# Kernel tuning notes

Measured on AMD Instinct MI355X. Metric: run time of the kernel, lower is better.

The kernel has to match this reference:

```python
import jax, jax.numpy as jnp
import numpy as np

B, C, H, W_ = 64, 512, 32, 32


def setup_inputs() -> dict:
    key = jax.random.key(0)
    k0, k1, k2, k3 = jax.random.split(key, 4)
    x = jax.random.normal(k0, (B, C, H, W_), dtype=jnp.float32)
    # conv1x1 weight [3c, c] (kernel dims of size 1 squeezed)
    W = jax.random.normal(k1, (3 * C, C), dtype=jnp.float32) * 0.02
    rel_h = jax.random.normal(k2, (1, C, H, 1), dtype=jnp.float32)
    rel_w = jax.random.normal(k3, (1, C, 1, W_), dtype=jnp.float32)
    return {"x": x, "W": W, "rel_h": rel_h, "rel_w": rel_w}


def reference(x, W, rel_h, rel_w):
    b, c, h, w = x.shape
    n = h * w
    xf = x.reshape(b, c, n)
    # 1x1 conv == channel matmul: [b, 3c, n]
    qkv = jnp.einsum('oc,bcn->bon', W, xf)
    q, k, v = jnp.split(qkv, 3, axis=1)  # each [b, c, n]
    # content-content: q^T k -> [b, n, n]
    content_content = jnp.einsum('bcn,bcm->bnm', q, k)
    # relative position bias: pos [c, n]; pos^T @ q -> [b, n, n]
    pos = (rel_h + rel_w).reshape(c, n)
    content_position = jnp.einsum('cn,bcm->bnm', pos, q)
    attention = jax.nn.softmax(content_content + content_position, axis=-1)
    # out = bmm(v, attention^T) -> [b, c, n]
    out = jnp.einsum('bcm,bnm->bcn', v, attention)
    return out.reshape(b, c, h, w)
```

## Files before the change

kernel.cpp:

```cpp
#include <hip/hip_runtime.h>

#define B_    64
#define C_    512
#define H_    32
#define WDIM  32
#define N_    1024
#define M3C   1536

typedef unsigned short ushort_t;
typedef __attribute__((ext_vector_type(8))) short bf16x8;
typedef __attribute__((ext_vector_type(4))) float f32x4;
typedef __attribute__((ext_vector_type(16))) float f32x16;

#define MEMFENCE asm volatile("" ::: "memory")

__device__ __forceinline__ ushort_t f2bf(float x) {
    unsigned u = __float_as_uint(x);
    unsigned r = (u + 0x7FFFu + ((u >> 16) & 1u)) >> 16;
    return (ushort_t)r;
}
__device__ __forceinline__ float bf2f(ushort_t b) {
    return __uint_as_float(((unsigned)b) << 16);
}
__device__ __forceinline__ void split_write(float v, ushort_t* __restrict__ ph,
                                            ushort_t* __restrict__ pl, size_t idx) {
    ushort_t hb = f2bf(v);
    ph[idx] = hb;
    pl[idx] = f2bf(v - bf2f(hb));
}

__device__ __forceinline__ void gld16(const void* g, void* l) {
    __builtin_amdgcn_global_load_lds((const __attribute__((address_space(1))) unsigned int*)g,
                                     (__attribute__((address_space(3))) unsigned int*)l,
                                     16, 0, 0);
}

__global__ __launch_bounds__(256) void pos_kernel(const float* __restrict__ rel_h,
                                                  const float* __restrict__ rel_w,
                                                  float* __restrict__ pos) {
    int idx = blockIdx.x * 256 + threadIdx.x;
    if (idx >= C_ * N_) return;
    int c = idx >> 10;
    int n = idx & (N_ - 1);
    int h = n >> 5;
    int w = n & (WDIM - 1);
    pos[idx] = rel_h[c * H_ + h] + rel_w[c * WDIM + w];
}

__global__ __launch_bounds__(256) void mmT_f32(const float* __restrict__ A, int lda,
                                               const float* __restrict__ B, int ldb,
                                               float* __restrict__ D, int ldd, int K) {
    __shared__ float As[16][64];
    __shared__ float Bs[16][64];
    const int m0 = blockIdx.y * 64;
    const int n0 = blockIdx.x * 64;
    const int tx = threadIdx.x, ty = threadIdx.y;
    const int tid = ty * 16 + tx;
    float acc[4][4] = {};
    for (int k0 = 0; k0 < K; k0 += 16) {
        #pragma unroll
        for (int t = 0; t < 4; ++t) {
            int e = tid + t * 256;
            int j = e >> 6, i = e & 63;
            As[j][i] = A[(size_t)(k0 + j) * lda + m0 + i];
            Bs[j][i] = B[(size_t)(k0 + j) * ldb + n0 + i];
        }
        __syncthreads();
        #pragma unroll
        for (int kk = 0; kk < 16; ++kk) {
            float a[4], bb[4];
            #pragma unroll
            for (int i = 0; i < 4; ++i) a[i]  = As[kk][ty * 4 + i];
            #pragma unroll
            for (int j = 0; j < 4; ++j) bb[j] = Bs[kk][tx * 4 + j];
            #pragma unroll
            for (int i = 0; i < 4; ++i)
                #pragma unroll
                for (int j = 0; j < 4; ++j)
                    acc[i][j] += a[i] * bb[j];
        }
        __syncthreads();
    }
    #pragma unroll
    for (int i = 0; i < 4; ++i)
        #pragma unroll
        for (int j = 0; j < 4; ++j)
            D[(size_t)(m0 + ty * 4 + i) * ldd + n0 + tx * 4 + j] = acc[i][j];
}

__global__ __launch_bounds__(256) void f_split(const float* __restrict__ Mtmp,
                                               const float* __restrict__ Wm,
                                               ushort_t* __restrict__ Fh,
                                               ushort_t* __restrict__ Fl) {
    int idx = blockIdx.x * 256 + threadIdx.x;
    if (idx >= 1024 * C_) return;
    int o = idx >> 9;
    int c = idx & (C_ - 1);
    float v = (o < 512) ? Mtmp[idx] : Wm[(size_t)(512 + o) * C_ + c];
    split_write(v, Fh, Fl, idx);
}

__global__ __launch_bounds__(256) void xT_split(const float* __restrict__ x,
                                                ushort_t* __restrict__ xh,
                                                ushort_t* __restrict__ xl) {
    __shared__ float t[32][33];
    const int bl = blockIdx.z;
    const int c0 = blockIdx.y * 32;
    const int n0 = blockIdx.x * 32;
    const float* xb = x + (size_t)bl * C_ * N_;
    ushort_t* xhb = xh + (size_t)bl * N_ * C_;
    ushort_t* xlb = xl + (size_t)bl * N_ * C_;
    const int tx = threadIdx.x & 31, ty = threadIdx.x >> 5;
    #pragma unroll
    for (int r = 0; r < 4; ++r)
        t[ty + r * 8][tx] = xb[(size_t)(c0 + ty + r * 8) * N_ + n0 + tx];
    __syncthreads();
    #pragma unroll
    for (int r = 0; r < 4; ++r) {
        float v = t[tx][ty + r * 8];
        size_t o = (size_t)(n0 + ty + r * 8) * C_ + c0 + tx;
        split_write(v, xhb, xlb, o);
    }
}


__global__ __launch_bounds__(512, 2) void g1_mfma(const ushort_t* __restrict__ Fh_,
                                                  const ushort_t* __restrict__ Fl_,
                                                  const ushort_t* __restrict__ xTh_,
                                                  const ushort_t* __restrict__ xTl_,
                                                  ushort_t* __restrict__ tTh_,
                                                  ushort_t* __restrict__ tTl_,
                                                  ushort_t* __restrict__ vh_,
                                                  ushort_t* __restrict__ vl_) {
    __shared__ ushort_t lds[2][4][2][4096];
    const int bl = blockIdx.z;
    const int n0 = blockIdx.x * 256;
    const int m0 = blockIdx.y * 256;
    const char* Ah = (const char*)Fh_;
    const char* Al = (const char*)Fl_;
    const char* Bh = (const char*)(xTh_ + (size_t)bl * N_ * C_);
    const char* Bl = (const char*)(xTl_ + (size_t)bl * N_ * C_);

    const int tid = threadIdx.x;
    const int lane = tid & 63, wid = tid >> 6;
    const int wr = wid >> 2, wc = wid & 3;
    const int l31 = lane & 31, l5 = lane >> 5;
    const int swz4 = (l31 >> 1) & 3;
    const int chk0 = ((l5)     ^ swz4) << 3;
    const int chk1 = ((2 | l5) ^ swz4) << 3;
    const int srow = tid >> 2;
    const int toff = srow * 1024 + (((tid & 3) ^ ((srow >> 1) & 3)) << 4);
    const int ldst = wid * 512;

    f32x16 acc[4][2] = {};

#define G1_ISSUE(buf, kb) \
    gld16(Ah + (size_t)(m0)       * 1024 + (kb) + toff, &lds[buf][0][0][ldst]); \
    gld16(Ah + (size_t)(m0 + 128) * 1024 + (kb) + toff, &lds[buf][0][1][ldst]); \
    gld16(Al + (size_t)(m0)       * 1024 + (kb) + toff, &lds[buf][1][0][ldst]); \
    gld16(Al + (size_t)(m0 + 128) * 1024 + (kb) + toff, &lds[buf][1][1][ldst]); \
    gld16(Bh + (size_t)(n0)       * 1024 + (kb) + toff, &lds[buf][2][0][ldst]); \
    gld16(Bh + (size_t)(n0 + 128) * 1024 + (kb) + toff, &lds[buf][2][1][ldst]); \
    gld16(Bl + (size_t)(n0)       * 1024 + (kb) + toff, &lds[buf][3][0][ldst]); \
    gld16(Bl + (size_t)(n0 + 128) * 1024 + (kb) + toff, &lds[buf][3][1][ldst]);

    G1_ISSUE(0, 0);
    G1_ISSUE(1, 64);
    int cur = 0;
    for (int t = 0; t < 16; ++t) {
        if (t + 1 < 16) asm volatile("s_waitcnt vmcnt(8)" ::: "memory");
        else            asm volatile("s_waitcnt vmcnt(0)" ::: "memory");
        __builtin_amdgcn_s_barrier();
        MEMFENCE;
        bf16x8 bh[2][2], bo[2][2];
        #pragma unroll
        for (int j = 0; j < 2; ++j) {
            int br = ((wc & 1) * 64 + j * 32 + l31) * 32;
            bh[j][0] = *(const bf16x8*)&lds[cur][2][wc >> 1][br + chk0];
            bh[j][1] = *(const bf16x8*)&lds[cur][2][wc >> 1][br + chk1];
            bo[j][0] = *(const bf16x8*)&lds[cur][3][wc >> 1][br + chk0];
            bo[j][1] = *(const bf16x8*)&lds[cur][3][wc >> 1][br + chk1];
        }
        #pragma unroll
        for (int i = 0; i < 4; ++i) {
            int ar = (i * 32 + l31) * 32;
            bf16x8 ah0 = *(const bf16x8*)&lds[cur][0][wr][ar + chk0];
            bf16x8 ah1 = *(const bf16x8*)&lds[cur][0][wr][ar + chk1];
            bf16x8 al0 = *(const bf16x8*)&lds[cur][1][wr][ar + chk0];
            bf16x8 al1 = *(const bf16x8*)&lds[cur][1][wr][ar + chk1];
            __builtin_amdgcn_s_setprio(1);
            #pragma unroll
            for (int j = 0; j < 2; ++j) {
                acc[i][j] = __builtin_amdgcn_mfma_f32_32x32x16_bf16(ah0, bh[j][0], acc[i][j], 0,0,0);
                acc[i][j] = __builtin_amdgcn_mfma_f32_32x32x16_bf16(ah0, bo[j][0], acc[i][j], 0,0,0);
                acc[i][j] = __builtin_amdgcn_mfma_f32_32x32x16_bf16(al0, bh[j][0], acc[i][j], 0,0,0);
                acc[i][j] = __builtin_amdgcn_mfma_f32_32x32x16_bf16(ah1, bh[j][1], acc[i][j], 0,0,0);
                acc[i][j] = __builtin_amdgcn_mfma_f32_32x32x16_bf16(ah1, bo[j][1], acc[i][j], 0,0,0);
                acc[i][j] = __builtin_amdgcn_mfma_f32_32x32x16_bf16(al1, bh[j][1], acc[i][j], 0,0,0);
            }
            __builtin_amdgcn_s_setprio(0);
        }
        asm volatile("s_waitcnt lgkmcnt(0)" ::: "memory");
        __builtin_amdgcn_sched_barrier(0);
        __builtin_amdgcn_s_barrier();
        MEMFENCE;
        if (t + 2 < 16) { G1_ISSUE(cur, (t + 2) * 64); }
        cur ^= 1;
    }
#undef G1_ISSUE

    if (m0 < 512) {
        ushort_t* th = tTh_ + (size_t)bl * N_ * C_;
        ushort_t* tl = tTl_ + (size_t)bl * N_ * C_;
        #pragma unroll
        for (int i = 0; i < 4; ++i)
            #pragma unroll
            for (int j = 0; j < 2; ++j) {
                int n = n0 + wc * 64 + j * 32 + l31;
                #pragma unroll
                for (int q = 0; q < 4; ++q) {
                    int o = m0 + wr * 128 + i * 32 + q * 8 + l5 * 4;
                    ushort4 h4, l4;
                    ushort_t hb;
                    float v0 = acc[i][j][q*4+0], v1 = acc[i][j][q*4+1];
                    float v2 = acc[i][j][q*4+2], v3 = acc[i][j][q*4+3];
                    hb = f2bf(v0); h4.x = hb; l4.x = f2bf(v0 - bf2f(hb));
                    hb = f2bf(v1); h4.y = hb; l4.y = f2bf(v1 - bf2f(hb));
                    hb = f2bf(v2); h4.z = hb; l4.z = f2bf(v2 - bf2f(hb));
                    hb = f2bf(v3); h4.w = hb; l4.w = f2bf(v3 - bf2f(hb));
                    *reinterpret_cast<ushort4*>(&th[(size_t)n * C_ + o]) = h4;
                    *reinterpret_cast<ushort4*>(&tl[(size_t)n * C_ + o]) = l4;
                }
            }
    } else {
        ushort_t* vh = vh_ + (size_t)bl * C_ * N_;
        ushort_t* vl = vl_ + (size_t)bl * C_ * N_;
        #pragma unroll
        for (int i = 0; i < 4; ++i)
            #pragma unroll
            for (int j = 0; j < 2; ++j) {
                int m = n0 + wc * 64 + j * 32 + l31;
                #pragma unroll
                for (int q = 0; q < 4; ++q) {
                    int cb = m0 - 512 + wr * 128 + i * 32 + q * 8 + l5 * 4;
                    #pragma unroll
                    for (int rr = 0; rr < 4; ++rr) {
                        float v = acc[i][j][q*4+rr];
                        ushort_t hb = f2bf(v);
                        vh[(size_t)(cb + rr) * N_ + m] = hb;
                        vl[(size_t)(cb + rr) * N_ + m] = f2bf(v - bf2f(hb));
                    }
                }
            }
    }
}

__global__ __launch_bounds__(512, 2) void g2_mfma(const ushort_t* __restrict__ xTh_,
                                                  const ushort_t* __restrict__ xTl_,
                                                  const ushort_t* __restrict__ rTh_,
                                                  const ushort_t* __restrict__ rTl_,
                                                  const ushort_t* __restrict__ tTh_,
                                                  const ushort_t* __restrict__ tTl_,
                                                  float* __restrict__ S) {
    __shared__ ushort_t lds[2][4][2][4096];
    const int bl = blockIdx.z;
    const int m0 = blockIdx.x * 256;
    const int n0 = blockIdx.y * 256;
    const char* xh = (const char*)(xTh_ + (size_t)bl * N_ * C_);
    const char* xl = (const char*)(xTl_ + (size_t)bl * N_ * C_);
    const char* th = (const char*)(tTh_ + (size_t)bl * N_ * C_);
    const char* tl = (const char*)(tTl_ + (size_t)bl * N_ * C_);
    const char* rh = (const char*)rTh_;
    const char* rl = (const char*)rTl_;

    const int tid = threadIdx.x;
    const int lane = tid & 63, wid = tid >> 6;
    const int wr = wid >> 2, wc = wid & 3;
    const int l31 = lane & 31, l5 = lane >> 5;
    const int swz4 = (l31 >> 1) & 3;
    const int chk0 = ((l5)     ^ swz4) << 3;
    const int chk1 = ((2 | l5) ^ swz4) << 3;
    const int srow = tid >> 2;
    const int toff = srow * 1024 + (((tid & 3) ^ ((srow >> 1) & 3)) << 4);
    const int ldst = wid * 512;

    f32x16 acc[4][2] = {};

#define G2_ISSUE(buf, pAh, pAl, pBh, pBl, kb) \
    gld16(pAh + (size_t)(n0)       * 1024 + (kb) + toff, &lds[buf][0][0][ldst]); \
    gld16(pAh + (size_t)(n0 + 128) * 1024 + (kb) + toff, &lds[buf][0][1][ldst]); \
    gld16(pAl + (size_t)(n0)       * 1024 + (kb) + toff, &lds[buf][1][0][ldst]); \
    gld16(pAl + (size_t)(n0 + 128) * 1024 + (kb) + toff, &lds[buf][1][1][ldst]); \
    gld16(pBh + (size_t)(m0)       * 1024 + (kb) + toff, &lds[buf][2][0][ldst]); \
    gld16(pBh + (size_t)(m0 + 128) * 1024 + (kb) + toff, &lds[buf][2][1][ldst]); \
    gld16(pBl + (size_t)(m0)       * 1024 + (kb) + toff, &lds[buf][3][0][ldst]); \
    gld16(pBl + (size_t)(m0 + 128) * 1024 + (kb) + toff, &lds[buf][3][1][ldst]);

    G2_ISSUE(0, xh, xl, th, tl, 0);
    G2_ISSUE(1, xh, xl, th, tl, 64);
    int cur = 0;
    for (int t = 0; t < 32; ++t) {
        if (t + 1 < 32) asm volatile("s_waitcnt vmcnt(8)" ::: "memory");
        else            asm volatile("s_waitcnt vmcnt(0)" ::: "memory");
        __builtin_amdgcn_s_barrier();
        MEMFENCE;
        bf16x8 bh[2][2], bo[2][2];
        #pragma unroll
        for (int j = 0; j < 2; ++j) {
            int br = ((wc & 1) * 64 + j * 32 + l31) * 32;
            bh[j][0] = *(const bf16x8*)&lds[cur][2][wc >> 1][br + chk0];
            bh[j][1] = *(const bf16x8*)&lds[cur][2][wc >> 1][br + chk1];
            bo[j][0] = *(const bf16x8*)&lds[cur][3][wc >> 1][br + chk0];
            bo[j][1] = *(const bf16x8*)&lds[cur][3][wc >> 1][br + chk1];
        }
        #pragma unroll
        for (int i = 0; i < 4; ++i) {
            int ar = (i * 32 + l31) * 32;
            bf16x8 ah0 = *(const bf16x8*)&lds[cur][0][wr][ar + chk0];
            bf16x8 ah1 = *(const bf16x8*)&lds[cur][0][wr][ar + chk1];
            bf16x8 al0 = *(const bf16x8*)&lds[cur][1][wr][ar + chk0];
            bf16x8 al1 = *(const bf16x8*)&lds[cur][1][wr][ar + chk1];
            __builtin_amdgcn_s_setprio(1);
            #pragma unroll
            for (int j = 0; j < 2; ++j) {
                acc[i][j] = __builtin_amdgcn_mfma_f32_32x32x16_bf16(ah0, bh[j][0], acc[i][j], 0,0,0);
                acc[i][j] = __builtin_amdgcn_mfma_f32_32x32x16_bf16(ah0, bo[j][0], acc[i][j], 0,0,0);
                acc[i][j] = __builtin_amdgcn_mfma_f32_32x32x16_bf16(al0, bh[j][0], acc[i][j], 0,0,0);
                acc[i][j] = __builtin_amdgcn_mfma_f32_32x32x16_bf16(ah1, bh[j][1], acc[i][j], 0,0,0);
                acc[i][j] = __builtin_amdgcn_mfma_f32_32x32x16_bf16(ah1, bo[j][1], acc[i][j], 0,0,0);
                acc[i][j] = __builtin_amdgcn_mfma_f32_32x32x16_bf16(al1, bh[j][1], acc[i][j], 0,0,0);
            }
            __builtin_amdgcn_s_setprio(0);
        }
        asm volatile("s_waitcnt lgkmcnt(0)" ::: "memory");
        __builtin_amdgcn_sched_barrier(0);
        __builtin_amdgcn_s_barrier();
        MEMFENCE;
        if (t + 2 < 32) {
            int s = t + 2;
            const char* pAh = (s < 16) ? xh : rh;
            const char* pAl = (s < 16) ? xl : rl;
            const char* pBh = (s < 16) ? th : xh;
            const char* pBl = (s < 16) ? tl : xl;
            int kb = (s & 15) * 64;
            G2_ISSUE(cur, pAh, pAl, pBh, pBl, kb);
        }
        cur ^= 1;
    }
#undef G2_ISSUE

    float* Sb = S + (size_t)bl * N_ * N_;
    #pragma unroll
    for (int i = 0; i < 4; ++i)
        #pragma unroll
        for (int j = 0; j < 2; ++j) {
            int m = m0 + wc * 64 + j * 32 + l31;
            #pragma unroll
            for (int q = 0; q < 4; ++q) {
                int n = n0 + wr * 128 + i * 32 + q * 8 + l5 * 4;
                #pragma unroll
                for (int rr = 0; rr < 4; ++rr)
                    Sb[(size_t)(n + rr) * N_ + m] = acc[i][j][q*4+rr];
            }
        }
}

__device__ __forceinline__ float waveMax(float v) {
    #pragma unroll
    for (int o = 32; o > 0; o >>= 1) v = fmaxf(v, __shfl_down(v, o));
    return v;
}
__device__ __forceinline__ float waveSum(float v) {
    #pragma unroll
    for (int o = 32; o > 0; o >>= 1) v += __shfl_down(v, o);
    return v;
}

__global__ __launch_bounds__(256) void softmax_bf16(const float* __restrict__ S,
                                                    ushort_t* __restrict__ P) {
    const float* Sr = S + (size_t)blockIdx.x * N_;
    ushort_t* Pr = P + (size_t)blockIdx.x * N_;
    const int tid = threadIdx.x;
    float4 v = reinterpret_cast<const float4*>(Sr)[tid];
    __shared__ float redm[4];
    __shared__ float reds[4];
    const int wave = tid >> 6, lane = tid & 63;

    float m = fmaxf(fmaxf(v.x, v.y), fmaxf(v.z, v.w));
    m = waveMax(m);
    if (lane == 0) redm[wave] = m;
    __syncthreads();
    m = fmaxf(fmaxf(redm[0], redm[1]), fmaxf(redm[2], redm[3]));

    v.x = __expf(v.x - m); v.y = __expf(v.y - m);
    v.z = __expf(v.z - m); v.w = __expf(v.w - m);
    float s = v.x + v.y + v.z + v.w;
    s = waveSum(s);
    if (lane == 0) reds[wave] = s;
    __syncthreads();
    s = reds[0] + reds[1] + reds[2] + reds[3];
    const float inv = 1.0f / s;
    ushort4 p;
    p.x = f2bf(v.x * inv); p.y = f2bf(v.y * inv);
    p.z = f2bf(v.z * inv); p.w = f2bf(v.w * inv);
    reinterpret_cast<ushort4*>(Pr)[tid] = p;
}

__global__ __launch_bounds__(512, 2) void g4_mfma(const ushort_t* __restrict__ vh_,
                                                  const ushort_t* __restrict__ vl_,
                                                  const ushort_t* __restrict__ P_,
                                                  float* __restrict__ out) {
    __shared__ ushort_t lds[2][3][2][4096];
    const int bl = blockIdx.z;
    const int n0 = blockIdx.x * 256;
    const int c0 = blockIdx.y * 256;
    const char* Ah = (const char*)(vh_ + (size_t)bl * C_ * N_);
    const char* Al = (const char*)(vl_ + (size_t)bl * C_ * N_);
    const char* Bp = (const char*)(P_ + (size_t)bl * N_ * N_);

    const int tid = threadIdx.x;
    const int lane = tid & 63, wid = tid >> 6;
    const int wr = wid >> 2, wc = wid & 3;
    const int l31 = lane & 31, l5 = lane >> 5;
    const int swz4 = (l31 >> 1) & 3;
    const int chk0 = ((l5)     ^ swz4) << 3;
    const int chk1 = ((2 | l5) ^ swz4) << 3;
    const int srow = tid >> 2;
    const int toff = srow * 2048 + (((tid & 3) ^ ((srow >> 1) & 3)) << 4);
    const int ldst = wid * 512;

    f32x16 acc[4][2] = {};

#define G4_ISSUE(buf, kb) \
    gld16(Ah + (size_t)(c0)       * 2048 + (kb) + toff, &lds[buf][0][0][ldst]); \
    gld16(Ah + (size_t)(c0 + 128) * 2048 + (kb) + toff, &lds[buf][0][1][ldst]); \
    gld16(Al + (size_t)(c0)       * 2048 + (kb) + toff, &lds[buf][1][0][ldst]); \
    gld16(Al + (size_t)(c0 + 128) * 2048 + (kb) + toff, &lds[buf][1][1][ldst]); \
    gld16(Bp + (size_t)(n0)       * 2048 + (kb) + toff, &lds[buf][2][0][ldst]); \
    gld16(Bp + (size_t)(n0 + 128) * 2048 + (kb) + toff, &lds[buf][2][1][ldst]);

    G4_ISSUE(0, 0);
    G4_ISSUE(1, 64);
    int cur = 0;
    for (int t = 0; t < 32; ++t) {
        if (t + 1 < 32) asm volatile("s_waitcnt vmcnt(6)" ::: "memory");
        else            asm volatile("s_waitcnt vmcnt(0)" ::: "memory");
        __builtin_amdgcn_s_barrier();
        MEMFENCE;
        bf16x8 bf[2][2];
        #pragma unroll
        for (int j = 0; j < 2; ++j) {
            int br = ((wc & 1) * 64 + j * 32 + l31) * 32;
            bf[j][0] = *(const bf16x8*)&lds[cur][2][wc >> 1][br + chk0];
            bf[j][1] = *(const bf16x8*)&lds[cur][2][wc >> 1][br + chk1];
        }
        #pragma unroll
        for (int i = 0; i < 4; ++i) {
            int ar = (i * 32 + l31) * 32;
            bf16x8 ah0 = *(const bf16x8*)&lds[cur][0][wr][ar + chk0];
            bf16x8 ah1 = *(const bf16x8*)&lds[cur][0][wr][ar + chk1];
            bf16x8 al0 = *(const bf16x8*)&lds[cur][1][wr][ar + chk0];
            bf16x8 al1 = *(const bf16x8*)&lds[cur][1][wr][ar + chk1];
            __builtin_amdgcn_s_setprio(1);
            #pragma unroll
            for (int j = 0; j < 2; ++j) {
                acc[i][j] = __builtin_amdgcn_mfma_f32_32x32x16_bf16(ah0, bf[j][0], acc[i][j], 0,0,0);
                acc[i][j] = __builtin_amdgcn_mfma_f32_32x32x16_bf16(al0, bf[j][0], acc[i][j], 0,0,0);
                acc[i][j] = __builtin_amdgcn_mfma_f32_32x32x16_bf16(ah1, bf[j][1], acc[i][j], 0,0,0);
                acc[i][j] = __builtin_amdgcn_mfma_f32_32x32x16_bf16(al1, bf[j][1], acc[i][j], 0,0,0);
            }
            __builtin_amdgcn_s_setprio(0);
        }
        asm volatile("s_waitcnt lgkmcnt(0)" ::: "memory");
        __builtin_amdgcn_sched_barrier(0);
        __builtin_amdgcn_s_barrier();
        MEMFENCE;
        if (t + 2 < 32) { G4_ISSUE(cur, (t + 2) * 64); }
        cur ^= 1;
    }
#undef G4_ISSUE

    float* ob = out + (size_t)bl * C_ * N_;
    #pragma unroll
    for (int i = 0; i < 4; ++i)
        #pragma unroll
        for (int j = 0; j < 2; ++j) {
            int n = n0 + wc * 64 + j * 32 + l31;
            #pragma unroll
            for (int q = 0; q < 4; ++q) {
                int c = c0 + wr * 128 + i * 32 + q * 8 + l5 * 4;
                #pragma unroll
                for (int rr = 0; rr < 4; ++rr)
                    ob[(size_t)(c + rr) * N_ + n] = acc[i][j][q*4+rr];
            }
        }
}

extern "C" void kernel_launch(void* const* d_in, const int* in_sizes, int n_in,
                              void* d_out, int out_size, void* d_ws, size_t ws_size,
                              hipStream_t stream) {
    const float* x     = (const float*)d_in[0];
    const float* Wm    = (const float*)d_in[1];
    const float* rel_h = (const float*)d_in[2];
    const float* rel_w = (const float*)d_in[3];
    float* out = (float*)d_out;

    const size_t posB  = (size_t)C_ * N_ * 4;
    const size_t MtB   = (size_t)C_ * C_ * 4;
    const size_t rtB   = (size_t)C_ * N_ * 4;
    const size_t fplB  = (size_t)1024 * C_ * 2;
    const size_t rtplB = (size_t)N_ * C_ * 2;
    const size_t xtB   = (size_t)N_ * C_ * 2;
    const size_t ttB   = (size_t)N_ * C_ * 2;
    const size_t vplB  = (size_t)C_ * N_ * 2;
    const size_t sB    = (size_t)N_ * N_ * 4;
    const size_t pB    = (size_t)N_ * N_ * 2;
    const size_t per_batch = 2 * xtB + 2 * ttB + 2 * vplB + sB + pB;
    const size_t persist   = posB + MtB + rtB + 2 * fplB + 2 * rtplB;

    size_t rem = (ws_size > persist) ? (ws_size - persist) : 0;
    int chunkB = (int)(rem / per_batch);
    if (chunkB < 1)  chunkB = 1;
    if (chunkB > B_) chunkB = B_;

    char* p = (char*)d_ws;
    float*    pos  = (float*)p;    p += posB;
    float*    Mtmp = (float*)p;    p += MtB;
    float*    rtmp = (float*)p;    p += rtB;
    ushort_t* Fh   = (ushort_t*)p; p += fplB;
    ushort_t* Fl   = (ushort_t*)p; p += fplB;
    ushort_t* rTh  = (ushort_t*)p; p += rtplB;
    ushort_t* rTl  = (ushort_t*)p; p += rtplB;
    ushort_t* xTh  = (ushort_t*)p; p += (size_t)chunkB * xtB;
    ushort_t* xTl  = (ushort_t*)p; p += (size_t)chunkB * xtB;
    ushort_t* tTh  = (ushort_t*)p; p += (size_t)chunkB * ttB;
    ushort_t* tTl  = (ushort_t*)p; p += (size_t)chunkB * ttB;
    ushort_t* vh   = (ushort_t*)p; p += (size_t)chunkB * vplB;
    ushort_t* vl   = (ushort_t*)p; p += (size_t)chunkB * vplB;
    float*    S    = (float*)p;    p += (size_t)chunkB * sB;
    ushort_t* P    = (ushort_t*)p; p += (size_t)chunkB * pB;

    dim3 blk16(16, 16);
    pos_kernel<<<(C_ * N_ + 255) / 256, 256, 0, stream>>>(rel_h, rel_w, pos);
    mmT_f32<<<dim3(C_ / 64, C_ / 64), blk16, 0, stream>>>(Wm, C_, Wm + (size_t)C_ * C_, C_,
                                                          Mtmp, C_, C_);
    mmT_f32<<<dim3(N_ / 64, C_ / 64), blk16, 0, stream>>>(Wm, C_, pos, N_, rtmp, N_, C_);
    f_split<<<(1024 * C_ + 255) / 256, 256, 0, stream>>>(Mtmp, Wm, Fh, Fl);
    xT_split<<<dim3(N_ / 32, C_ / 32, 1), 256, 0, stream>>>(rtmp, rTh, rTl);

    for (int b0 = 0; b0 < B_; b0 += chunkB) {
        int nb = (b0 + chunkB <= B_) ? chunkB : (B_ - b0);
        const float* x_b   = x   + (size_t)b0 * C_ * N_;
        float*       out_b = out + (size_t)b0 * C_ * N_;
        xT_split<<<dim3(N_ / 32, C_ / 32, nb), 256, 0, stream>>>(x_b, xTh, xTl);
        g1_mfma<<<dim3(4, 4, nb), 512, 0, stream>>>(Fh, Fl, xTh, xTl, tTh, tTl, vh, vl);
        g2_mfma<<<dim3(4, 4, nb), 512, 0, stream>>>(xTh, xTl, rTh, rTl, tTh, tTl, S);
        softmax_bf16<<<nb * N_, 256, 0, stream>>>(S, P);
        g4_mfma<<<dim3(4, 2, nb), 512, 0, stream>>>(vh, vl, P, out_b);
    }
}
```

Baseline: 1.332 ms.

## Restructure split-bf16 GEMM mainloops into 4-phase 128-wide-K pipeline with 16x16 MFMA

Rewrites the three split-precision GEMM kernels so each K step is 128 wide and is split into four quadrant phases. Each phase issues the next staging load (6 stages in flight) and then runs 16x16x32 MFMAs on one 128x128 quadrant. The hi/lo split terms are now serialised along the K dimension as segments instead of being issued as paired MFMAs. The goal is finer-grained overlap of global-to-LDS loads with compute and fewer barriers per FLOP, with an XOR swizzle over 8 chunks to avoid LDS bank conflicts. The costs are a more complex wait schedule and different MFMA shapes and accumulator layout.

Result: slower. 1.759 ms (+32.0%).

```diff
diff --git a/kernel.cpp b/kernel.cpp
--- a/kernel.cpp
+++ b/kernel.cpp
@@ -10,7 +10,6 @@
 typedef unsigned short ushort_t;
 typedef __attribute__((ext_vector_type(8))) short bf16x8;
 typedef __attribute__((ext_vector_type(4))) float f32x4;
-typedef __attribute__((ext_vector_type(16))) float f32x16;
 
 #define MEMFENCE asm volatile("" ::: "memory")
 
@@ -124,6 +123,49 @@
 }
 
 
+#define STAGE2(srcp, gstride, r0, kb, dstp) \
+    _Pragma("unroll") \
+    for (int s_ = 0; s_ < 2; ++s_) { \
+        int row_ = s_ * 64 + (tid >> 3); \
+        gld16((srcp) + (size_t)((r0) + row_) * (gstride) + (kb) + \
+                  (((tid & 7) ^ (row_ & 7)) << 4), \
+              (dstp) + s_ * 4096 + (wid << 9)); \
+    }
+
+#define PHASE_WAIT(t_, q_, TT) \
+    if ((t_) < (TT) - 1) asm volatile("s_waitcnt vmcnt(8)" ::: "memory"); \
+    else if ((q_) == 0)  asm volatile("s_waitcnt vmcnt(4)" ::: "memory"); \
+    else if ((q_) == 1)  asm volatile("s_waitcnt vmcnt(2)" ::: "memory"); \
+    else                 asm volatile("s_waitcnt vmcnt(0)" ::: "memory");
+
+#define PHASE_COMPUTE(buf_, qr_, qc_, q_) \
+    bf16x8 af_[4][2], bf_[2][2]; \
+    _Pragma("unroll") \
+    for (int i_ = 0; i_ < 4; ++i_) { \
+        int row_ = wr * 64 + i_ * 16 + lr; \
+        const ushort_t* ab_ = &ldsA[buf_][qr_][row_ * 64]; \
+        af_[i_][0] = *(const bf16x8*)&ab_[((g ^ (row_ & 7)) << 3)]; \
+        af_[i_][1] = *(const bf16x8*)&ab_[(((4 + g) ^ (row_ & 7)) << 3)]; \
+    } \
+    _Pragma("unroll") \
+    for (int j_ = 0; j_ < 2; ++j_) { \
+        int row_ = wc * 32 + j_ * 16 + lr; \
+        const ushort_t* bb_ = &ldsB[buf_][qc_][row_ * 64]; \
+        bf_[j_][0] = *(const bf16x8*)&bb_[((g ^ (row_ & 7)) << 3)]; \
+        bf_[j_][1] = *(const bf16x8*)&bb_[(((4 + g) ^ (row_ & 7)) << 3)]; \
+    } \
+    asm volatile("s_waitcnt lgkmcnt(0)" ::: "memory"); \
+    __builtin_amdgcn_sched_barrier(0); \
+    __builtin_amdgcn_s_setprio(1); \
+    _Pragma("unroll") \
+    for (int i_ = 0; i_ < 4; ++i_) \
+        _Pragma("unroll") \
+        for (int j_ = 0; j_ < 2; ++j_) { \
+            acc[q_][i_][j_] = __builtin_amdgcn_mfma_f32_16x16x32_bf16(af_[i_][0], bf_[j_][0], acc[q_][i_][j_], 0, 0, 0); \
+            acc[q_][i_][j_] = __builtin_amdgcn_mfma_f32_16x16x32_bf16(af_[i_][1], bf_[j_][1], acc[q_][i_][j_], 0, 0, 0); \
+        } \
+    __builtin_amdgcn_s_setprio(0);
+
 __global__ __launch_bounds__(512, 2) void g1_mfma(const ushort_t* __restrict__ Fh_,
                                                   const ushort_t* __restrict__ Fl_,
                                                   const ushort_t* __restrict__ xTh_,
@@ -132,98 +174,73 @@
                                                   ushort_t* __restrict__ tTl_,
                                                   ushort_t* __restrict__ vh_,
                                                   ushort_t* __restrict__ vl_) {
-    __shared__ ushort_t lds[2][4][2][4096];
+    __shared__ ushort_t ldsA[2][2][8192];
+    __shared__ ushort_t ldsB[2][2][8192];
     const int bl = blockIdx.z;
     const int n0 = blockIdx.x * 256;
     const int m0 = blockIdx.y * 256;
-    const char* Ah = (const char*)Fh_;
-    const char* Al = (const char*)Fl_;
-    const char* Bh = (const char*)(xTh_ + (size_t)bl * N_ * C_);
-    const char* Bl = (const char*)(xTl_ + (size_t)bl * N_ * C_);
+    const char* fh = (const char*)Fh_;
+    const char* fl = (const char*)Fl_;
+    const char* xh = (const char*)(xTh_ + (size_t)bl * N_ * C_);
+    const char* xl = (const char*)(xTl_ + (size_t)bl * N_ * C_);
 
     const int tid = threadIdx.x;
     const int lane = tid & 63, wid = tid >> 6;
     const int wr = wid >> 2, wc = wid & 3;
-    const int l31 = lane & 31, l5 = lane >> 5;
-    const int swz4 = (l31 >> 1) & 3;
-    const int chk0 = ((l5)     ^ swz4) << 3;
-    const int chk1 = ((2 | l5) ^ swz4) << 3;
-    const int srow = tid >> 2;
-    const int toff = srow * 1024 + (((tid & 3) ^ ((srow >> 1) & 3)) << 4);
-    const int ldst = wid * 512;
-
-    f32x16 acc[4][2] = {};
-
-#define G1_ISSUE(buf, kb) \
-    gld16(Ah + (size_t)(m0)       * 1024 + (kb) + toff, &lds[buf][0][0][ldst]); \
-    gld16(Ah + (size_t)(m0 + 128) * 1024 + (kb) + toff, &lds[buf][0][1][ldst]); \
-    gld16(Al + (size_t)(m0)       * 1024 + (kb) + toff, &lds[buf][1][0][ldst]); \
-    gld16(Al + (size_t)(m0 + 128) * 1024 + (kb) + toff, &lds[buf][1][1][ldst]); \
-    gld16(Bh + (size_t)(n0)       * 1024 + (kb) + toff, &lds[buf][2][0][ldst]); \
-    gld16(Bh + (size_t)(n0 + 128) * 1024 + (kb) + toff, &lds[buf][2][1][ldst]); \
-    gld16(Bl + (size_t)(n0)       * 1024 + (kb) + toff, &lds[buf][3][0][ldst]); \
-    gld16(Bl + (size_t)(n0 + 128) * 1024 + (kb) + toff, &lds[buf][3][1][ldst]);
-
-    G1_ISSUE(0, 0);
-    G1_ISSUE(1, 64);
-    int cur = 0;
-    for (int t = 0; t < 16; ++t) {
-        if (t + 1 < 16) asm volatile("s_waitcnt vmcnt(8)" ::: "memory");
-        else            asm volatile("s_waitcnt vmcnt(0)" ::: "memory");
-        __builtin_amdgcn_s_barrier();
-        MEMFENCE;
-        bf16x8 bh[2][2], bo[2][2];
-        #pragma unroll
-        for (int j = 0; j < 2; ++j) {
-            int br = ((wc & 1) * 64 + j * 32 + l31) * 32;
-            bh[j][0] = *(const bf16x8*)&lds[cur][2][wc >> 1][br + chk0];
-            bh[j][1] = *(const bf16x8*)&lds[cur][2][wc >> 1][br + chk1];
-            bo[j][0] = *(const bf16x8*)&lds[cur][3][wc >> 1][br + chk0];
-            bo[j][1] = *(const bf16x8*)&lds[cur][3][wc >> 1][br + chk1];
-        }
-        #pragma unroll
-        for (int i = 0; i < 4; ++i) {
-            int ar = (i * 32 + l31) * 32;
-            bf16x8 ah0 = *(const bf16x8*)&lds[cur][0][wr][ar + chk0];
-            bf16x8 ah1 = *(const bf16x8*)&lds[cur][0][wr][ar + chk1];
-            bf16x8 al0 = *(const bf16x8*)&lds[cur][1][wr][ar + chk0];
-            bf16x8 al1 = *(const bf16x8*)&lds[cur][1][wr][ar + chk1];
-            __builtin_amdgcn_s_setprio(1);
-            #pragma unroll
-            for (int j = 0; j < 2; ++j) {
-                acc[i][j] = __builtin_amdgcn_mfma_f32_32x32x16_bf16(ah0, bh[j][0], acc[i][j], 0,0,0);
-                acc[i][j] = __builtin_amdgcn_mfma_f32_32x32x16_bf16(ah0, bo[j][0], acc[i][j], 0,0,0);
-                acc[i][j] = __builtin_amdgcn_mfma_f32_32x32x16_bf16(al0, bh[j][0], acc[i][j], 0,0,0);
-                acc[i][j] = __builtin_amdgcn_mfma_f32_32x32x16_bf16(ah1, bh[j][1], acc[i][j], 0,0,0);
-                acc[i][j] = __builtin_amdgcn_mfma_f32_32x32x16_bf16(ah1, bo[j][1], acc[i][j], 0,0,0);
-                acc[i][j] = __builtin_amdgcn_mfma_f32_32x32x16_bf16(al1, bh[j][1], acc[i][j], 0,0,0);
-            }
-            __builtin_amdgcn_s_setprio(0);
-        }
-        asm volatile("s_waitcnt lgkmcnt(0)" ::: "memory");
-        __builtin_amdgcn_sched_barrier(0);
-        __builtin_amdgcn_s_barrier();
-        MEMFENCE;
-        if (t + 2 < 16) { G1_ISSUE(cur, (t + 2) * 64); }
-        cur ^= 1;
-    }
-#undef G1_ISSUE
+    const int lr = lane & 15, g = lane >> 4;
+    const int T = 24;
+
+    f32x4 acc[4][4][2] = {};
+
+#define G1_STAGE(h_) do { \
+    int th_ = (h_) >> 2, kind_ = (h_) & 3, bu_ = th_ & 1; \
+    int seg_ = th_ >> 3, kb_ = (th_ & 7) * 128; \
+    if (kind_ == 0 || kind_ == 3) { \
+        int hf_ = (kind_ == 3); \
+        const char* s_p = (seg_ == 2) ? fl : fh; \
+        STAGE2(s_p, 1024, m0 + hf_ * 128, kb_, &ldsA[bu_][hf_][0]); \
+    } else { \
+        int hf_ = (kind_ == 2); \
+        const char* s_p = (seg_ == 1) ? xl : xh; \
+        STAGE2(s_p, 1024, n0 + hf_ * 128, kb_, &ldsB[bu_][hf_][0]); \
+    } \
+} while (0)
+
+#define G1_PHASE(t_, q_, qr_, qc_) do { \
+    PHASE_WAIT(t_, q_, T); \
+    __builtin_amdgcn_s_barrier(); \
+    MEMFENCE; \
+    { int h_ = 4 * (t_) + (q_) + 6; if (h_ < 4 * T) G1_STAGE(h_); } \
+    const int bu_ = (t_) & 1; \
+    PHASE_COMPUTE(bu_, qr_, qc_, q_); \
+} while (0)
+
+    #pragma unroll
+    for (int h = 0; h < 6; ++h) G1_STAGE(h);
+    for (int t = 0; t < T; ++t) {
+        G1_PHASE(t, 0, 0, 0);
+        G1_PHASE(t, 1, 0, 1);
+        G1_PHASE(t, 2, 1, 0);
+        G1_PHASE(t, 3, 1, 1);
+    }
+#undef G1_PHASE
+#undef G1_STAGE
 
     if (m0 < 512) {
         ushort_t* th = tTh_ + (size_t)bl * N_ * C_;
         ushort_t* tl = tTl_ + (size_t)bl * N_ * C_;
         #pragma unroll
-        for (int i = 0; i < 4; ++i)
-            #pragma unroll
-            for (int j = 0; j < 2; ++j) {
-                int n = n0 + wc * 64 + j * 32 + l31;
+        for (int q = 0; q < 4; ++q)
+            #pragma unroll
+            for (int i = 0; i < 4; ++i)
                 #pragma unroll
-                for (int q = 0; q < 4; ++q) {
-                    int o = m0 + wr * 128 + i * 32 + q * 8 + l5 * 4;
+                for (int j = 0; j < 2; ++j) {
+                    int o = m0 + (q >> 1) * 128 + wr * 64 + i * 16 + g * 4;
+                    int n = n0 + (q & 1) * 128 + wc * 32 + j * 16 + lr;
                     ushort4 h4, l4;
                     ushort_t hb;
-                    float v0 = acc[i][j][q*4+0], v1 = acc[i][j][q*4+1];
-                    float v2 = acc[i][j][q*4+2], v3 = acc[i][j][q*4+3];
+                    float v0 = acc[q][i][j][0], v1 = acc[q][i][j][1];
+                    float v2 = acc[q][i][j][2], v3 = acc[q][i][j][3];
                     hb = f2bf(v0); h4.x = hb; l4.x = f2bf(v0 - bf2f(hb));
                     hb = f2bf(v1); h4.y = hb; l4.y = f2bf(v1 - bf2f(hb));
                     hb = f2bf(v2); h4.z = hb; l4.z = f2bf(v2 - bf2f(hb));
@@ -231,27 +248,25 @@
                     *reinterpret_cast<ushort4*>(&th[(size_t)n * C_ + o]) = h4;
                     *reinterpret_cast<ushort4*>(&tl[(size_t)n * C_ + o]) = l4;
                 }
-            }
     } else {
         ushort_t* vh = vh_ + (size_t)bl * C_ * N_;
         ushort_t* vl = vl_ + (size_t)bl * C_ * N_;
         #pragma unroll
-        for (int i = 0; i < 4; ++i)
-            #pragma unroll
-            for (int j = 0; j < 2; ++j) {
-                int m = n0 + wc * 64 + j * 32 + l31;
+        for (int q = 0; q < 4; ++q)
+            #pragma unroll
+            for (int i = 0; i < 4; ++i)
                 #pragma unroll
-                for (int q = 0; q < 4; ++q) {
-                    int cb = m0 - 512 + wr * 128 + i * 32 + q * 8 + l5 * 4;
+                for (int j = 0; j < 2; ++j) {
+                    int cb = m0 - 512 + (q >> 1) * 128 + wr * 64 + i * 16 + g * 4;
+                    int m = n0 + (q & 1) * 128 + wc * 32 + j * 16 + lr;
                     #pragma unroll
                     for (int rr = 0; rr < 4; ++rr) {
-                        float v = acc[i][j][q*4+rr];
+                        float v = acc[q][i][j][rr];
                         ushort_t hb = f2bf(v);
                         vh[(size_t)(cb + rr) * N_ + m] = hb;
                         vl[(size_t)(cb + rr) * N_ + m] = f2bf(v - bf2f(hb));
                     }
                 }
-            }
     }
 }
 
@@ -262,7 +277,8 @@
                                                   const ushort_t* __restrict__ tTh_,
                                                   const ushort_t* __restrict__ tTl_,
                                                   float* __restrict__ S) {
-    __shared__ ushort_t lds[2][4][2][4096];
+    __shared__ ushort_t ldsA[2][2][8192];
+    __shared__ ushort_t ldsB[2][2][8192];
     const int bl = blockIdx.z;
     const int m0 = blockIdx.x * 256;
     const int n0 = blockIdx.y * 256;
@@ -276,93 +292,60 @@
     const int tid = threadIdx.x;
     const int lane = tid & 63, wid = tid >> 6;
     const int wr = wid >> 2, wc = wid & 3;
-    const int l31 = lane & 31, l5 = lane >> 5;
-    const int swz4 = (l31 >> 1) & 3;
-    const int chk0 = ((l5)     ^ swz4) << 3;
-    const int chk1 = ((2 | l5) ^ swz4) << 3;
-    const int srow = tid >> 2;
-    const int toff = srow * 1024 + (((tid & 3) ^ ((srow >> 1) & 3)) << 4);
-    const int ldst = wid * 512;
-
-    f32x16 acc[4][2] = {};
-
-#define G2_ISSUE(buf, pAh, pAl, pBh, pBl, kb) \
-    gld16(pAh + (size_t)(n0)       * 1024 + (kb) + toff, &lds[buf][0][0][ldst]); \
-    gld16(pAh + (size_t)(n0 + 128) * 1024 + (kb) + toff, &lds[buf][0][1][ldst]); \
-    gld16(pAl + (size_t)(n0)       * 1024 + (kb) + toff, &lds[buf][1][0][ldst]); \
-    gld16(pAl + (size_t)(n0 + 128) * 1024 + (kb) + toff, &lds[buf][1][1][ldst]); \
-    gld16(pBh + (size_t)(m0)       * 1024 + (kb) + toff, &lds[buf][2][0][ldst]); \
-    gld16(pBh + (size_t)(m0 + 128) * 1024 + (kb) + toff, &lds[buf][2][1][ldst]); \
-    gld16(pBl + (size_t)(m0)       * 1024 + (kb) + toff, &lds[buf][3][0][ldst]); \
-    gld16(pBl + (size_t)(m0 + 128) * 1024 + (kb) + toff, &lds[buf][3][1][ldst]);
-
-    G2_ISSUE(0, xh, xl, th, tl, 0);
-    G2_ISSUE(1, xh, xl, th, tl, 64);
-    int cur = 0;
-    for (int t = 0; t < 32; ++t) {
-        if (t + 1 < 32) asm volatile("s_waitcnt vmcnt(8)" ::: "memory");
-        else            asm volatile("s_waitcnt vmcnt(0)" ::: "memory");
-        __builtin_amdgcn_s_barrier();
-        MEMFENCE;
-        bf16x8 bh[2][2], bo[2][2];
-        #pragma unroll
-        for (int j = 0; j < 2; ++j) {
-            int br = ((wc & 1) * 64 + j * 32 + l31) * 32;
-            bh[j][0] = *(const bf16x8*)&lds[cur][2][wc >> 1][br + chk0];
-            bh[j][1] = *(const bf16x8*)&lds[cur][2][wc >> 1][br + chk1];
-            bo[j][0] = *(const bf16x8*)&lds[cur][3][wc >> 1][br + chk0];
-            bo[j][1] = *(const bf16x8*)&lds[cur][3][wc >> 1][br + chk1];
-        }
-        #pragma unroll
-        for (int i = 0; i < 4; ++i) {
-            int ar = (i * 32 + l31) * 32;
-            bf16x8 ah0 = *(const bf16x8*)&lds[cur][0][wr][ar + chk0];
-            bf16x8 ah1 = *(const bf16x8*)&lds[cur][0][wr][ar + chk1];
-            bf16x8 al0 = *(const bf16x8*)&lds[cur][1][wr][ar + chk0];
-            bf16x8 al1 = *(const bf16x8*)&lds[cur][1][wr][ar + chk1];
-            __builtin_amdgcn_s_setprio(1);
+    const int lr = lane & 15, g = lane >> 4;
+    const int T = 48;
+
+    f32x4 acc[4][4][2] = {};
+
+#define G2_STAGE(h_) do { \
+    int th_ = (h_) >> 2, kind_ = (h_) & 3, bu_ = th_ & 1; \
+    int seg_ = th_ >> 3, kb_ = (th_ & 7) * 128; \
+    if (kind_ == 0 || kind_ == 3) { \
+        int hf_ = (kind_ == 3); \
+        const char* s_p = (seg_ < 3) ? ((seg_ == 2) ? xl : xh) \
+                                     : ((seg_ == 5) ? rl : rh); \
+        STAGE2(s_p, 1024, n0 + hf_ * 128, kb_, &ldsA[bu_][hf_][0]); \
+    } else { \
+        int hf_ = (kind_ == 2); \
+        const char* s_p = (seg_ < 3) ? ((seg_ == 1) ? tl : th) \
+                                     : ((seg_ == 4) ? xl : xh); \
+        STAGE2(s_p, 1024, m0 + hf_ * 128, kb_, &ldsB[bu_][hf_][0]); \
+    } \
+} while (0)
+
+#define G2_PHASE(t_, q_, qr_, qc_) do { \
+    PHASE_WAIT(t_, q_, T); \
+    __builtin_amdgcn_s_barrier(); \
+    MEMFENCE; \
+    { int h_ = 4 * (t_) + (q_) + 6; if (h_ < 4 * T) G2_STAGE(h_); } \
+    const int bu_ = (t_) & 1; \
+    PHASE_COMPUTE(bu_, qr_, qc_, q_); \
+} while (0)
+
+    #pragma unroll
+    for (int h = 0; h < 6; ++h) G2_STAGE(h);
+    for (int t = 0; t < T; ++t) {
+        G2_PHASE(t, 0, 0, 0);
+        G2_PHASE(t, 1, 0, 1);
+        G2_PHASE(t, 2, 1, 0);
+        G2_PHASE(t, 3, 1, 1);
+    }
+#undef G2_PHASE
+#undef G2_STAGE
+
+    float* Sb = S + (size_t)bl * N_ * N_;
+    #pragma unroll
+    for (int q = 0; q < 4; ++q)
+        #pragma unroll
+        for (int i = 0; i < 4; ++i)
             #pragma unroll
             for (int j = 0; j < 2; ++j) {
-                acc[i][j] = __builtin_amdgcn_mfma_f32_32x32x16_bf16(ah0, bh[j][0], acc[i][j], 0,0,0);
-                acc[i][j] = __builtin_amdgcn_mfma_f32_32x32x16_bf16(ah0, bo[j][0], acc[i][j], 0,0,0);
-                acc[i][j] = __builtin_amdgcn_mfma_f32_32x32x16_bf16(al0, bh[j][0], acc[i][j], 0,0,0);
-                acc[i][j] = __builtin_amdgcn_mfma_f32_32x32x16_bf16(ah1, bh[j][1], acc[i][j], 0,0,0);
-                acc[i][j] = __builtin_amdgcn_mfma_f32_32x32x16_bf16(ah1, bo[j][1], acc[i][j], 0,0,0);
-                acc[i][j] = __builtin_amdgcn_mfma_f32_32x32x16_bf16(al1, bh[j][1], acc[i][j], 0,0,0);
-            }
-            __builtin_amdgcn_s_setprio(0);
-        }
-        asm volatile("s_waitcnt lgkmcnt(0)" ::: "memory");
-        __builtin_amdgcn_sched_barrier(0);
-        __builtin_amdgcn_s_barrier();
-        MEMFENCE;
-        if (t + 2 < 32) {
-            int s = t + 2;
-            const char* pAh = (s < 16) ? xh : rh;
-            const char* pAl = (s < 16) ? xl : rl;
-            const char* pBh = (s < 16) ? th : xh;
-            const char* pBl = (s < 16) ? tl : xl;
-            int kb = (s & 15) * 64;
-            G2_ISSUE(cur, pAh, pAl, pBh, pBl, kb);
-        }
-        cur ^= 1;
-    }
-#undef G2_ISSUE
-
-    float* Sb = S + (size_t)bl * N_ * N_;
-    #pragma unroll
-    for (int i = 0; i < 4; ++i)
-        #pragma unroll
-        for (int j = 0; j < 2; ++j) {
-            int m = m0 + wc * 64 + j * 32 + l31;
-            #pragma unroll
-            for (int q = 0; q < 4; ++q) {
-                int n = n0 + wr * 128 + i * 32 + q * 8 + l5 * 4;
+                int n = n0 + (q >> 1) * 128 + wr * 64 + i * 16 + g * 4;
+                int m = m0 + (q & 1) * 128 + wc * 32 + j * 16 + lr;
                 #pragma unroll
                 for (int rr = 0; rr < 4; ++rr)
-                    Sb[(size_t)(n + rr) * N_ + m] = acc[i][j][q*4+rr];
+                    Sb[(size_t)(n + rr) * N_ + m] = acc[q][i][j][rr];
             }
-        }
 }
 
 __device__ __forceinline__ float waveMax(float v) {
@@ -410,90 +393,69 @@
                                                   const ushort_t* __restrict__ vl_,
                                                   const ushort_t* __restrict__ P_,
                                                   float* __restrict__ out) {
-    __shared__ ushort_t lds[2][3][2][4096];
+    __shared__ ushort_t ldsA[2][2][8192];
+    __shared__ ushort_t ldsB[2][2][8192];
     const int bl = blockIdx.z;
     const int n0 = blockIdx.x * 256;
     const int c0 = blockIdx.y * 256;
-    const char* Ah = (const char*)(vh_ + (size_t)bl * C_ * N_);
-    const char* Al = (const char*)(vl_ + (size_t)bl * C_ * N_);
-    const char* Bp = (const char*)(P_ + (size_t)bl * N_ * N_);
+    const char* avh = (const char*)(vh_ + (size_t)bl * C_ * N_);
+    const char* avl = (const char*)(vl_ + (size_t)bl * C_ * N_);
+    const char* bp  = (const char*)(P_ + (size_t)bl * N_ * N_);
 
     const int tid = threadIdx.x;
     const int lane = tid & 63, wid = tid >> 6;
     const int wr = wid >> 2, wc = wid & 3;
-    const int l31 = lane & 31, l5 = lane >> 5;
-    const int swz4 = (l31 >> 1) & 3;
-    const int chk0 = ((l5)     ^ swz4) << 3;
-    const int chk1 = ((2 | l5) ^ swz4) << 3;
-    const int srow = tid >> 2;
-    const int toff = srow * 2048 + (((tid & 3) ^ ((srow >> 1) & 3)) << 4);
-    const int ldst = wid * 512;
-
-    f32x16 acc[4][2] = {};
-
-#define G4_ISSUE(buf, kb) \
-    gld16(Ah + (size_t)(c0)       * 2048 + (kb) + toff, &lds[buf][0][0][ldst]); \
-    gld16(Ah + (size_t)(c0 + 128) * 2048 + (kb) + toff, &lds[buf][0][1][ldst]); \
-    gld16(Al + (size_t)(c0)       * 2048 + (kb) + toff, &lds[buf][1][0][ldst]); \
-    gld16(Al + (size_t)(c0 + 128) * 2048 + (kb) + toff, &lds[buf][1][1][ldst]); \
-    gld16(Bp + (size_t)(n0)       * 2048 + (kb) + toff, &lds[buf][2][0][ldst]); \
-    gld16(Bp + (size_t)(n0 + 128) * 2048 + (kb) + toff, &lds[buf][2][1][ldst]);
-
-    G4_ISSUE(0, 0);
-    G4_ISSUE(1, 64);
-    int cur = 0;
-    for (int t = 0; t < 32; ++t) {
-        if (t + 1 < 32) asm volatile("s_waitcnt vmcnt(6)" ::: "memory");
-        else            asm volatile("s_waitcnt vmcnt(0)" ::: "memory");
-        __builtin_amdgcn_s_barrier();
-        MEMFENCE;
-        bf16x8 bf[2][2];
-        #pragma unroll
-        for (int j = 0; j < 2; ++j) {
-            int br = ((wc & 1) * 64 + j * 32 + l31) * 32;
-            bf[j][0] = *(const bf16x8*)&lds[cur][2][wc >> 1][br + chk0];
-            bf[j][1] = *(const bf16x8*)&lds[cur][2][wc >> 1][br + chk1];
-        }
-        #pragma unroll
-        for (int i = 0; i < 4; ++i) {
-            int ar = (i * 32 + l31) * 32;
-            bf16x8 ah0 = *(const bf16x8*)&lds[cur][0][wr][ar + chk0];
-            bf16x8 ah1 = *(const bf16x8*)&lds[cur][0][wr][ar + chk1];
-            bf16x8 al0 = *(const bf16x8*)&lds[cur][1][wr][ar + chk0];
-            bf16x8 al1 = *(const bf16x8*)&lds[cur][1][wr][ar + chk1];
-            __builtin_amdgcn_s_setprio(1);
+    const int lr = lane & 15, g = lane >> 4;
+    const int T = 32;
+
+    f32x4 acc[4][4][2] = {};
+
+#define G4_STAGE(h_) do { \
+    int th_ = (h_) >> 2, kind_ = (h_) & 3, bu_ = th_ & 1; \
+    int seg_ = th_ >> 4, kb_ = (th_ & 15) * 128; \
+    if (kind_ == 0 || kind_ == 3) { \
+        int hf_ = (kind_ == 3); \
+        const char* s_p = seg_ ? avl : avh; \
+        STAGE2(s_p, 2048, c0 + hf_ * 128, kb_, &ldsA[bu_][hf_][0]); \
+    } else { \
+        int hf_ = (kind_ == 2); \
+        STAGE2(bp, 2048, n0 + hf_ * 128, kb_, &ldsB[bu_][hf_][0]); \
+    } \
+} while (0)
+
+#define G4_PHASE(t_, q_, qr_, qc_) do { \
+    PHASE_WAIT(t_, q_, T); \
+    __builtin_amdgcn_s_barrier(); \
+    MEMFENCE; \
+    { int h_ = 4 * (t_) + (q_) + 6; if (h_ < 4 * T) G4_STAGE(h_); } \
+    const int bu_ = (t_) & 1; \
+    PHASE_COMPUTE(bu_, qr_, qc_, q_); \
+} while (0)
+
+    #pragma unroll
+    for (int h = 0; h < 6; ++h) G4_STAGE(h);
+    for (int t = 0; t < T; ++t) {
+        G4_PHASE(t, 0, 0, 0);
+        G4_PHASE(t, 1, 0, 1);
+        G4_PHASE(t, 2, 1, 0);
+        G4_PHASE(t, 3, 1, 1);
+    }
+#undef G4_PHASE
+#undef G4_STAGE
+
+    float* ob = out + (size_t)bl * C_ * N_;
+    #pragma unroll
+    for (int q = 0; q < 4; ++q)
+        #pragma unroll
+        for (int i = 0; i < 4; ++i)
             #pragma unroll
             for (int j = 0; j < 2; ++j) {
-                acc[i][j] = __builtin_amdgcn_mfma_f32_32x32x16_bf16(ah0, bf[j][0], acc[i][j], 0,0,0);
-                acc[i][j] = __builtin_amdgcn_mfma_f32_32x32x16_bf16(al0, bf[j][0], acc[i][j], 0,0,0);
-                acc[i][j] = __builtin_amdgcn_mfma_f32_32x32x16_bf16(ah1, bf[j][1], acc[i][j], 0,0,0);
-                acc[i][j] = __builtin_amdgcn_mfma_f32_32x32x16_bf16(al1, bf[j][1], acc[i][j], 0,0,0);
-            }
-            __builtin_amdgcn_s_setprio(0);
-        }
-        asm volatile("s_waitcnt lgkmcnt(0)" ::: "memory");
-        __builtin_amdgcn_sched_barrier(0);
-        __builtin_amdgcn_s_barrier();
-        MEMFENCE;
-        if (t + 2 < 32) { G4_ISSUE(cur, (t + 2) * 64); }
-        cur ^= 1;
-    }
-#undef G4_ISSUE
-
-    float* ob = out + (size_t)bl * C_ * N_;
-    #pragma unroll
-    for (int i = 0; i < 4; ++i)
-        #pragma unroll
-        for (int j = 0; j < 2; ++j) {
-            int n = n0 + wc * 64 + j * 32 + l31;
-            #pragma unroll
-            for (int q = 0; q < 4; ++q) {
-                int c = c0 + wr * 128 + i * 32 + q * 8 + l5 * 4;
+                int c = c0 + (q >> 1) * 128 + wr * 64 + i * 16 + g * 4;
+                int n = n0 + (q & 1) * 128 + wc * 32 + j * 16 + lr;
                 #pragma unroll
                 for (int rr = 0; rr < 4; ++rr)
-                    ob[(size_t)(c + rr) * N_ + n] = acc[i][j][q*4+rr];
+                    ob[(size_t)(c + rr) * N_ + n] = acc[q][i][j][rr];
             }
-        }
 }
 
 extern "C" void kernel_launch(void* const* d_in, const int* in_sizes, int n_in,
```
